# Kernel tuning notes

Hardware: AMD Instinct MI355X
Metric: run time of the kernel (lower is better)

The kernel has to match this reference:

```python
import jax, jax.numpy as jnp
import numpy as np

EPS = 1e-12  # keras K.l2_normalize epsilon


def _l2_normalize(v, axis):
    return v * jax.lax.rsqrt(jnp.maximum(jnp.sum(v * v, axis=axis, keepdims=True), EPS))


def setup_inputs() -> dict:
    key = jax.random.key(0)
    k1, k2, k3, k4 = jax.random.split(key, 4)
    B, T, D, K, O = 32, 1024, 512, 64, 1024
    x = jax.random.normal(k1, (B, T, D), dtype=jnp.float32)
    weight = jax.random.normal(k2, (D, K), dtype=jnp.float32) * (1.0 / np.sqrt(D))
    bias = jnp.zeros((K,), dtype=jnp.float32)
    centers = jax.random.normal(k3, (K, D), dtype=jnp.float32)
    reduc_dim = jax.random.normal(k4, (D * K, O), dtype=jnp.float32) * 0.01
    return {"x": x, "weight": weight, "bias": bias, "centers": centers, "reduc_dim": reduc_dim}


def reference(x, weight, bias, centers, reduc_dim):
    # x: [B,T,D], weight: [D,K], bias: [K]
    # soft assignment: softmax over centers
    a = jax.nn.softmax(jnp.einsum('btd,dk->btk', x, weight) + bias, axis=-1)  # [B,T,K]
    # aggregate descriptors per center: batch_dot over time axis -> [B,K,D]
    x_agg = jnp.einsum('btk,btd->bkd', a, x)
    # total soft weight per center: [B,K]
    sum_w = jnp.sum(a, axis=1)
    # residual vs centers, broadcast: [B,K,D]
    full = x_agg - sum_w[:, :, None] * centers[None, :, :]
    # intra-normalize per center vector
    full = _l2_normalize(full, axis=-1)
    B = x.shape[0]
    full = full.reshape(B, -1)  # [B, K*D]
    full = _l2_normalize(full, axis=-1)
    return full @ reduc_dim  # [B, output_dim]
```

## Files before the change

### kernel.cpp

```cpp
#include <hip/hip_runtime.h>
#include <math.h>

#define TT 1024
#define DD 512
#define KK 64
#define OO 1024
#define EPSF 1e-12f

typedef __attribute__((ext_vector_type(8))) short bf16x8;
typedef __attribute__((ext_vector_type(4))) float f32x4;

__device__ __forceinline__ ushort f2bf(float f) {
  unsigned u = __float_as_uint(f);
  u = (u + 0x7FFFu + ((u >> 16) & 1u)) >> 16;
  return (ushort)u;
}
__device__ __forceinline__ float bf2f(ushort h) {
  return __uint_as_float(((unsigned)h) << 16);
}


__global__ __launch_bounds__(256) void nv_k0(const float* __restrict__ w,
                                             ushort* __restrict__ whT,
                                             float* __restrict__ sum_w) {
  int idx = blockIdx.x * 256 + threadIdx.x;
  if (idx < 32768) {
    int d = idx >> 6, k = idx & 63;
    whT[(size_t)k * DD + d] = f2bf(w[idx]);
  } else if (idx < 32768 + 2048) {
    sum_w[idx - 32768] = 0.f;
  }
}

__global__ __launch_bounds__(512) void nv_k12(
    const float* __restrict__ x, const ushort* __restrict__ whT,
    const float* __restrict__ bias, float* __restrict__ xaggP,
    float* __restrict__ sum_w) {
  const int tsp = blockIdx.x, b = blockIdx.y;
  const int t0 = tsp * 128;
  const int tid = threadIdx.x;
  const int wave = tid >> 6, lane = tid & 63, l15 = lane & 15, q = lane >> 4;

  __shared__ ushort xT[512 * 128];
  __shared__ ushort aTl[64 * 128];

  f32x4 acc[4];
#pragma unroll
  for (int nt = 0; nt < 4; ++nt)
#pragma unroll
    for (int r = 0; r < 4; ++r) acc[nt][r] = 0.f;

  const int trow = wave * 16 + l15;
  const float* xrow = x + (size_t)(b * TT + t0 + trow) * DD;
  const int tg = trow >> 3, tlo = trow & 7;

  for (int dc = 0; dc < DD; dc += 64) {
#pragma unroll
    for (int kc = 0; kc < 2; ++kc) {
      const int dbase = dc + kc * 32 + q * 8;
      float4 v0 = *(const float4*)(xrow + dbase);
      float4 v1 = *(const float4*)(xrow + dbase + 4);
      bf16x8 af;
      af[0] = (short)f2bf(v0.x); af[1] = (short)f2bf(v0.y);
      af[2] = (short)f2bf(v0.z); af[3] = (short)f2bf(v0.w);
      af[4] = (short)f2bf(v1.x); af[5] = (short)f2bf(v1.y);
      af[6] = (short)f2bf(v1.z); af[7] = (short)f2bf(v1.w);
#pragma unroll
      for (int j = 0; j < 8; ++j) {
        const int d = dbase + j;
        xT[d * 128 + ((tg ^ (d & 15)) << 3) + tlo] = (ushort)af[j];
      }
      bf16x8 bfv[4];
#pragma unroll
      for (int nt = 0; nt < 4; ++nt)
        bfv[nt] = *(const bf16x8*)(whT + (size_t)(nt * 16 + l15) * DD + dbase);
#pragma unroll
      for (int nt = 0; nt < 4; ++nt)
        acc[nt] = __builtin_amdgcn_mfma_f32_16x16x32_bf16(af, bfv[nt], acc[nt], 0, 0, 0);
    }
  }

  float bia[4];
#pragma unroll
  for (int nt = 0; nt < 4; ++nt) bia[nt] = bias[nt * 16 + l15];

  ushort au[4][4];
  float sw[4] = {0.f, 0.f, 0.f, 0.f};
#pragma unroll
  for (int r = 0; r < 4; ++r) {
    float l[4];
#pragma unroll
    for (int nt = 0; nt < 4; ++nt) l[nt] = acc[nt][r] + bia[nt];
    float m = fmaxf(fmaxf(l[0], l[1]), fmaxf(l[2], l[3]));
#pragma unroll
    for (int s = 1; s <= 8; s <<= 1) m = fmaxf(m, __shfl_xor(m, s));
    float e[4];
#pragma unroll
    for (int nt = 0; nt < 4; ++nt) e[nt] = __expf(l[nt] - m);
    float ssum = e[0] + e[1] + e[2] + e[3];
#pragma unroll
    for (int s = 1; s <= 8; s <<= 1) ssum += __shfl_xor(ssum, s);
    float inv = 1.f / ssum;
#pragma unroll
    for (int nt = 0; nt < 4; ++nt) {
      ushort u = f2bf(e[nt] * inv);
      au[nt][r] = u;
      sw[nt] += bf2f(u);
    }
  }
#pragma unroll
  for (int nt = 0; nt < 4; ++nt) {
    float s = sw[nt];
    s += __shfl_xor(s, 16);
    s += __shfl_xor(s, 32);
    if (q == 0) atomicAdd(sum_w + b * KK + nt * 16 + l15, s);
  }
#pragma unroll
  for (int nt = 0; nt < 4; ++nt)
#pragma unroll
    for (int r = 0; r < 4; ++r) {
      const int k = nt * 16 + l15;
      const int t = wave * 16 + q * 4 + r;
      aTl[k * 128 + (((t >> 3) ^ (k & 15)) << 3) + (t & 7)] = au[nt][r];
    }
  __syncthreads();

  f32x4 accB[4][4];
#pragma unroll
  for (int mk = 0; mk < 4; ++mk)
#pragma unroll
    for (int nd = 0; nd < 4; ++nd)
#pragma unroll
      for (int r = 0; r < 4; ++r) accB[mk][nd][r] = 0.f;

#pragma unroll
  for (int kc = 0; kc < 4; ++kc) {
    const int g = kc * 4 + q;
    bf16x8 afr[4], bfr[4];
#pragma unroll
    for (int mk = 0; mk < 4; ++mk) {
      const int k = mk * 16 + l15;
      afr[mk] = *(const bf16x8*)(aTl + k * 128 + ((g ^ (k & 15)) << 3));
    }
#pragma unroll
    for (int nd = 0; nd < 4; ++nd) {
      const int d = wave * 64 + nd * 16 + l15;
      bfr[nd] = *(const bf16x8*)(xT + d * 128 + ((g ^ (d & 15)) << 3));
    }
#pragma unroll
    for (int mk = 0; mk < 4; ++mk)
#pragma unroll
      for (int nd = 0; nd < 4; ++nd)
        accB[mk][nd] =
            __builtin_amdgcn_mfma_f32_16x16x32_bf16(afr[mk], bfr[nd], accB[mk][nd], 0, 0, 0);
  }
#pragma unroll
  for (int mk = 0; mk < 4; ++mk)
#pragma unroll
    for (int nd = 0; nd < 4; ++nd)
#pragma unroll
      for (int r = 0; r < 4; ++r) {
        const int k = mk * 16 + q * 4 + r;
        const int d = wave * 64 + nd * 16 + l15;
        xaggP[(size_t)((tsp * 32 + b) * KK + k) * DD + d] = accB[mk][nd][r];
      }
}

__global__ __launch_bounds__(128) void nv_k3a(
    const float* __restrict__ xaggP, float* __restrict__ full,
    const float* __restrict__ centers, const float* __restrict__ sum_w,
    float* __restrict__ s1) {
  const int k = blockIdx.x, b = blockIdx.y;
  const int tid = threadIdx.x;
  const float sw = sum_w[b * KK + k];
  float4 v = make_float4(0.f, 0.f, 0.f, 0.f);
#pragma unroll
  for (int sp = 0; sp < 8; ++sp) {
    float4 p = *((const float4*)(xaggP + (size_t)((sp * 32 + b) * KK + k) * DD) + tid);
    v.x += p.x; v.y += p.y; v.z += p.z; v.w += p.w;
  }
  float4 c = *((const float4*)(centers + (size_t)k * DD) + tid);
  v.x = fmaf(-sw, c.x, v.x);
  v.y = fmaf(-sw, c.y, v.y);
  v.z = fmaf(-sw, c.z, v.z);
  v.w = fmaf(-sw, c.w, v.w);
  *((float4*)(full + (size_t)(b * KK + k) * DD) + tid) = v;
  float ss = v.x * v.x + v.y * v.y + v.z * v.z + v.w * v.w;
#pragma unroll
  for (int s = 1; s <= 32; s <<= 1) ss += __shfl_xor(ss, s);
  __shared__ float red[2];
  if ((tid & 63) == 0) red[tid >> 6] = ss;
  __syncthreads();
  if (tid == 0) s1[b * KK + k] = red[0] + red[1];
}

__global__ __launch_bounds__(64) void nv_k3b(const float* __restrict__ s1,
                                             float* __restrict__ scale) {
  const int b = blockIdx.x, k = threadIdx.x;
  float r = s1[b * KK + k];
  float d1 = fmaxf(r, EPSF);
  float s2 = r / d1;
#pragma unroll
  for (int s = 1; s <= 32; s <<= 1) s2 += __shfl_xor(s2, s);
  scale[b * KK + k] = rsqrtf(d1) * rsqrtf(fmaxf(s2, EPSF));
}

__global__ __launch_bounds__(256) void nv_k3c(const float* __restrict__ full,
                                              const float* __restrict__ scale,
                                              float* __restrict__ fullT) {
  const int k = blockIdx.x, d0 = blockIdx.y * 128;
  const int tid = threadIdx.x;
  __shared__ float ls[32 * 132];

#pragma unroll
  for (int it = 0; it < 4; ++it) {
    int fi = it * 256 + tid;
    int b = fi >> 5, dg = fi & 31;
    float sc = scale[b * KK + k];
    float4 v = *((const float4*)(full + (size_t)(b * KK + k) * DD + d0) + dg);
    v.x *= sc; v.y *= sc; v.z *= sc; v.w *= sc;
    *(float4*)(ls + b * 132 + dg * 4) = v;
  }
  __syncthreads();
#pragma unroll
  for (int it = 0; it < 4; ++it) {
    int fo = it * 256 + tid;
    int d = fo >> 3, bq = fo & 7;
    float4 v;
    v.x = ls[(bq * 4 + 0) * 132 + d];
    v.y = ls[(bq * 4 + 1) * 132 + d];
    v.z = ls[(bq * 4 + 2) * 132 + d];
    v.w = ls[(bq * 4 + 3) * 132 + d];
    *(float4*)(fullT + (size_t)(k * DD + d0 + d) * 32 + bq * 4) = v;
  }
}

__global__ __launch_bounds__(256) void nv_k4(
    const float* __restrict__ fullT, const float* __restrict__ reduc,
    float* __restrict__ outP) {
  const int strip = blockIdx.x;
  const int ksp = blockIdx.y;
  const int tid = threadIdx.x;
  const int wave = tid >> 6, lane = tid & 63;
  const int c0 = strip * 256 + lane * 4;
  const int kblk = ksp * 256;

  __shared__ float fst[256 * 32];

#pragma unroll
  for (int it = 0; it < 8; ++it) {
    int f4 = it * 256 + tid;
    *(float4*)(fst + f4 * 4) = *(const float4*)(fullT + (size_t)kblk * 32 + f4 * 4);
  }
  __syncthreads();

  float4 acc[32];
#pragma unroll
  for (int b = 0; b < 32; ++b) acc[b] = make_float4(0.f, 0.f, 0.f, 0.f);

  const int kw = wave * 64;
  for (int kk = 0; kk < 64; kk += 4) {
    float4 rv[4];
#pragma unroll
    for (int j = 0; j < 4; ++j)
      rv[j] = *(const float4*)(reduc + (size_t)(kblk + kw + kk + j) * OO + c0);
#pragma unroll
    for (int j = 0; j < 4; ++j) {
      const int kl = kw + kk + j;
#pragma unroll
      for (int b4 = 0; b4 < 8; ++b4) {
        float4 fv = *(const float4*)(fst + kl * 32 + b4 * 4);
        acc[b4 * 4 + 0].x = fmaf(fv.x, rv[j].x, acc[b4 * 4 + 0].x);
        acc[b4 * 4 + 0].y = fmaf(fv.x, rv[j].y, acc[b4 * 4 + 0].y);
        acc[b4 * 4 + 0].z = fmaf(fv.x, rv[j].z, acc[b4 * 4 + 0].z);
        acc[b4 * 4 + 0].w = fmaf(fv.x, rv[j].w, acc[b4 * 4 + 0].w);
        acc[b4 * 4 + 1].x = fmaf(fv.y, rv[j].x, acc[b4 * 4 + 1].x);
        acc[b4 * 4 + 1].y = fmaf(fv.y, rv[j].y, acc[b4 * 4 + 1].y);
        acc[b4 * 4 + 1].z = fmaf(fv.y, rv[j].z, acc[b4 * 4 + 1].z);
        acc[b4 * 4 + 1].w = fmaf(fv.y, rv[j].w, acc[b4 * 4 + 1].w);
        acc[b4 * 4 + 2].x = fmaf(fv.z, rv[j].x, acc[b4 * 4 + 2].x);
        acc[b4 * 4 + 2].y = fmaf(fv.z, rv[j].y, acc[b4 * 4 + 2].y);
        acc[b4 * 4 + 2].z = fmaf(fv.z, rv[j].z, acc[b4 * 4 + 2].z);
        acc[b4 * 4 + 2].w = fmaf(fv.z, rv[j].w, acc[b4 * 4 + 2].w);
        acc[b4 * 4 + 3].x = fmaf(fv.w, rv[j].x, acc[b4 * 4 + 3].x);
        acc[b4 * 4 + 3].y = fmaf(fv.w, rv[j].y, acc[b4 * 4 + 3].y);
        acc[b4 * 4 + 3].z = fmaf(fv.w, rv[j].z, acc[b4 * 4 + 3].z);
        acc[b4 * 4 + 3].w = fmaf(fv.w, rv[j].w, acc[b4 * 4 + 3].w);
      }
    }
  }

  __syncthreads();
  for (int w = 0; w < 4; ++w) {
    if (wave == w) {
      if (w == 0) {
#pragma unroll
        for (int b = 0; b < 32; ++b)
          *(float4*)(fst + b * 256 + lane * 4) = acc[b];
      } else {
#pragma unroll
        for (int b = 0; b < 32; ++b) {
          float4 v = *(float4*)(fst + b * 256 + lane * 4);
          v.x += acc[b].x; v.y += acc[b].y; v.z += acc[b].z; v.w += acc[b].w;
          *(float4*)(fst + b * 256 + lane * 4) = v;
        }
      }
    }
    __syncthreads();
  }

#pragma unroll
  for (int it = 0; it < 8; ++it) {
    int f4 = it * 256 + tid;
    int b = f4 >> 6, cg = f4 & 63;
    *(float4*)(outP + ((size_t)(ksp * 32 + b) * OO) + strip * 256 + cg * 4) =
        *(const float4*)(fst + b * 256 + cg * 4);
  }
}

__global__ __launch_bounds__(128) void nv_k5(const float* __restrict__ outP,
                                             float* __restrict__ out) {
  const int idx = blockIdx.x * 128 + threadIdx.x;
  float s = 0.f;
#pragma unroll 8
  for (int sp = 0; sp < 128; ++sp) s += outP[(size_t)sp * 32768 + idx];
  out[idx] = s;
}

extern "C" void kernel_launch(void* const* d_in, const int* in_sizes, int n_in,
                              void* d_out, int out_size, void* d_ws, size_t ws_size,
                              hipStream_t stream) {
  const float* x = (const float*)d_in[0];
  const float* weight = (const float*)d_in[1];
  const float* bias = (const float*)d_in[2];
  const float* centers = (const float*)d_in[3];
  const float* reduc = (const float*)d_in[4];
  float* out = (float*)d_out;
  float* ws = (float*)d_ws;

  float* xaggP = ws;
  float* full = ws + 8388608;
  float* fullT = ws + 9437184;
  float* outP = ws + 10485760;
  ushort* whT = (ushort*)(ws + 14680064);
  float* sum_w = ws + 14696448;
  float* s1 = sum_w + 2048;
  float* scale = sum_w + 4096;

  nv_k0<<<136, 256, 0, stream>>>(weight, whT, sum_w);
  nv_k12<<<dim3(8, 32), 512, 0, stream>>>(x, whT, bias, xaggP, sum_w);
  nv_k3a<<<dim3(64, 32), 128, 0, stream>>>(xaggP, full, centers, sum_w, s1);
  nv_k3b<<<32, 64, 0, stream>>>(s1, scale);
  nv_k3c<<<dim3(64, 4), 256, 0, stream>>>(full, scale, fullT);
  nv_k4<<<dim3(4, 128), 256, 0, stream>>>(fullT, reduc, outP);
  nv_k5<<<256, 128, 0, stream>>>(outP, out);
}
```

Baseline: 277.8 us.

## Stage x and weight tiles in LDS with coalesced loads; fold scale kernel into transpose

The first GEMM in nv_k12 now loads x tiles cooperatively with coalesced row-wise reads, converts them to bf16, and stores them in a swizzled LDS buffer (reused later for the assignment matrix). The weight tile also goes through LDS, so MFMA operands come from shared memory rather than strided global reads per lane. This adds two barriers per d-chunk and more LDS usage. Separately, the tiny nv_k3b launch is removed, and its global-norm scale is recomputed redundantly inside each nv_k3c block, saving one kernel launch.

```diff
diff --git a/kernel.cpp b/kernel.cpp
--- a/kernel.cpp
+++ b/kernel.cpp
@@ -42,7 +42,10 @@
   const int wave = tid >> 6, lane = tid & 63, l15 = lane & 15, q = lane >> 4;
 
   __shared__ ushort xT[512 * 128];
-  __shared__ ushort aTl[64 * 128];
+  __shared__ ushort xsa[128 * 64];
+  __shared__ ushort wsm[64 * 64];
+  ushort* xs = xsa;
+  ushort* aTl = xsa;
 
   f32x4 acc[4];
 #pragma unroll
@@ -50,34 +53,49 @@
 #pragma unroll
     for (int r = 0; r < 4; ++r) acc[nt][r] = 0.f;
 
-  const int trow = wave * 16 + l15;
-  const float* xrow = x + (size_t)(b * TT + t0 + trow) * DD;
-  const int tg = trow >> 3, tlo = trow & 7;
-
   for (int dc = 0; dc < DD; dc += 64) {
 #pragma unroll
+    for (int it = 0; it < 2; ++it) {
+      int gi = it * 512 + tid;
+      int t = gi >> 3, gd = gi & 7;
+      const float* px = x + (size_t)(b * TT + t0 + t) * DD + dc + gd * 8;
+      float4 v0 = *(const float4*)px;
+      float4 v1 = *(const float4*)(px + 4);
+      bf16x8 pk;
+      pk[0] = (short)f2bf(v0.x); pk[1] = (short)f2bf(v0.y);
+      pk[2] = (short)f2bf(v0.z); pk[3] = (short)f2bf(v0.w);
+      pk[4] = (short)f2bf(v1.x); pk[5] = (short)f2bf(v1.y);
+      pk[6] = (short)f2bf(v1.z); pk[7] = (short)f2bf(v1.w);
+      *(bf16x8*)(xs + t * 64 + ((gd ^ (t & 7)) << 3)) = pk;
+      const int tg = t >> 3, tlo = t & 7;
+#pragma unroll
+      for (int j = 0; j < 8; ++j) {
+        const int d = dc + gd * 8 + j;
+        xT[d * 128 + ((tg ^ (d & 15)) << 3) + tlo] = (ushort)pk[j];
+      }
+    }
+    {
+      int k = tid >> 3, gd = tid & 7;
+      bf16x8 v = *(const bf16x8*)(whT + (size_t)k * DD + dc + gd * 8);
+      *(bf16x8*)(wsm + k * 64 + ((gd ^ (k & 7)) << 3)) = v;
+    }
+    __syncthreads();
+#pragma unroll
     for (int kc = 0; kc < 2; ++kc) {
-      const int dbase = dc + kc * 32 + q * 8;
-      float4 v0 = *(const float4*)(xrow + dbase);
-      float4 v1 = *(const float4*)(xrow + dbase + 4);
-      bf16x8 af;
-      af[0] = (short)f2bf(v0.x); af[1] = (short)f2bf(v0.y);
-      af[2] = (short)f2bf(v0.z); af[3] = (short)f2bf(v0.w);
-      af[4] = (short)f2bf(v1.x); af[5] = (short)f2bf(v1.y);
-      af[6] = (short)f2bf(v1.z); af[7] = (short)f2bf(v1.w);
-#pragma unroll
-      for (int j = 0; j < 8; ++j) {
-        const int d = dbase + j;
-        xT[d * 128 + ((tg ^ (d & 15)) << 3) + tlo] = (ushort)af[j];
-      }
+      const int gq = kc * 4 + q;
       bf16x8 bfv[4];
 #pragma unroll
-      for (int nt = 0; nt < 4; ++nt)
-        bfv[nt] = *(const bf16x8*)(whT + (size_t)(nt * 16 + l15) * DD + dbase);
+      for (int nt = 0; nt < 4; ++nt) {
+        const int k = nt * 16 + l15;
+        bfv[nt] = *(const bf16x8*)(wsm + k * 64 + ((gq ^ (k & 7)) << 3));
+      }
+      const int t = wave * 16 + l15;
+      bf16x8 af = *(const bf16x8*)(xs + t * 64 + ((gq ^ (t & 7)) << 3));
 #pragma unroll
       for (int nt = 0; nt < 4; ++nt)
         acc[nt] = __builtin_amdgcn_mfma_f32_16x16x32_bf16(af, bfv[nt], acc[nt], 0, 0, 0);
     }
+    __syncthreads();
   }
 
   float bia[4];
@@ -115,6 +133,8 @@
     s += __shfl_xor(s, 32);
     if (q == 0) atomicAdd(sum_w + b * KK + nt * 16 + l15, s);
   }
+
+  __syncthreads();
 #pragma unroll
   for (int nt = 0; nt < 4; ++nt)
 #pragma unroll
@@ -194,29 +214,35 @@
   if (tid == 0) s1[b * KK + k] = red[0] + red[1];
 }
 
-__global__ __launch_bounds__(64) void nv_k3b(const float* __restrict__ s1,
-                                             float* __restrict__ scale) {
-  const int b = blockIdx.x, k = threadIdx.x;
-  float r = s1[b * KK + k];
-  float d1 = fmaxf(r, EPSF);
-  float s2 = r / d1;
-#pragma unroll
-  for (int s = 1; s <= 32; s <<= 1) s2 += __shfl_xor(s2, s);
-  scale[b * KK + k] = rsqrtf(d1) * rsqrtf(fmaxf(s2, EPSF));
-}
-
 __global__ __launch_bounds__(256) void nv_k3c(const float* __restrict__ full,
-                                              const float* __restrict__ scale,
+                                              const float* __restrict__ s1,
                                               float* __restrict__ fullT) {
   const int k = blockIdx.x, d0 = blockIdx.y * 128;
   const int tid = threadIdx.x;
   __shared__ float ls[32 * 132];
+  __shared__ float s2s[32];
+
+  {
+    int bb = tid >> 3, k8 = tid & 7;
+    float p = 0.f;
+#pragma unroll
+    for (int i = 0; i < 8; ++i) {
+      float r = s1[bb * KK + k8 * 8 + i];
+      p += r / fmaxf(r, EPSF);
+    }
+    p += __shfl_xor(p, 1);
+    p += __shfl_xor(p, 2);
+    p += __shfl_xor(p, 4);
+    if (k8 == 0) s2s[bb] = rsqrtf(fmaxf(p, EPSF));
+  }
+  __syncthreads();
 
 #pragma unroll
   for (int it = 0; it < 4; ++it) {
     int fi = it * 256 + tid;
     int b = fi >> 5, dg = fi & 31;
-    float sc = scale[b * KK + k];
+    float r = s1[b * KK + k];
+    float sc = rsqrtf(fmaxf(r, EPSF)) * s2s[b];
     float4 v = *((const float4*)(full + (size_t)(b * KK + k) * DD + d0) + dg);
     v.x *= sc; v.y *= sc; v.z *= sc; v.w *= sc;
     *(float4*)(ls + b * 132 + dg * 4) = v;
@@ -345,13 +371,11 @@
   ushort* whT = (ushort*)(ws + 14680064);
   float* sum_w = ws + 14696448;
   float* s1 = sum_w + 2048;
-  float* scale = sum_w + 4096;
 
   nv_k0<<<136, 256, 0, stream>>>(weight, whT, sum_w);
   nv_k12<<<dim3(8, 32), 512, 0, stream>>>(x, whT, bias, xaggP, sum_w);
   nv_k3a<<<dim3(64, 32), 128, 0, stream>>>(xaggP, full, centers, sum_w, s1);
-  nv_k3b<<<32, 64, 0, stream>>>(s1, scale);
-  nv_k3c<<<dim3(64, 4), 256, 0, stream>>>(full, scale, fullT);
+  nv_k3c<<<dim3(64, 4), 256, 0, stream>>>(full, s1, fullT);
   nv_k4<<<dim3(4, 128), 256, 0, stream>>>(fullT, reduc, outP);
   nv_k5<<<256, 128, 0, stream>>>(outP, out);
 }
```

New measurement: 275.2 us. No clear change (-1.0%).
